# Kernel tuning notes

Hardware: AMD Instinct MI355X
Metric: run time of the kernel (lower is better)

Reference implementation:

```python
import jax, jax.numpy as jnp
import numpy as np

B, N, IN_DIM, OUT_DIM, H = 8, 1024, 256, 256, 4
HD = OUT_DIM // H  # head_dim = 64
NEG = -1e9
EPS = 1e-5


def setup_inputs() -> dict:
    key = jax.random.key(0)
    ks = jax.random.split(key, 9)
    h = jax.random.normal(ks[0], (B, N, IN_DIM), dtype=jnp.float32)
    adj = jax.random.randint(ks[1], (N, N), 0, 2, dtype=jnp.int32)
    adj = adj.at[jnp.arange(N), jnp.arange(N)].set(1)  # self loops so no empty rows
    s = 1.0 / np.sqrt(IN_DIM)
    W = jax.random.uniform(ks[2], (H, IN_DIM, HD), jnp.float32, -s, s)
    sa = 1.0 / np.sqrt(2 * HD)
    a1 = jax.random.uniform(ks[3], (H, HD), jnp.float32, -sa, sa)
    a2 = jax.random.uniform(ks[4], (H, HD), jnp.float32, -sa, sa)
    sp = 1.0 / np.sqrt(OUT_DIM)
    proj_w = jax.random.uniform(ks[5], (OUT_DIM, OUT_DIM), jnp.float32, -sp, sp)
    proj_b = jax.random.uniform(ks[6], (OUT_DIM,), jnp.float32, -sp, sp)
    gamma = jnp.ones((OUT_DIM,), jnp.float32)
    beta = jnp.zeros((OUT_DIM,), jnp.float32)
    return {"h": h, "adj": adj, "W": W, "a1": a1, "a2": a2,
            "proj_w": proj_w, "proj_b": proj_b, "gamma": gamma, "beta": beta}


def reference(h, adj, W, a1, a2, proj_w, proj_b, gamma, beta):
    # Wh: [B,H,N,HD]
    Wh = jnp.einsum('bni,hid->bhnd', h, W)
    # Decompose a([Wh_i || Wh_j]) = a1.Wh_i + a2.Wh_j (same math as concat+linear)
    si = jnp.einsum('bhnd,hd->bhn', Wh, a1)  # [B,H,N]
    sj = jnp.einsum('bhnd,hd->bhn', Wh, a2)
    e = jax.nn.leaky_relu(si[:, :, :, None] + sj[:, :, None, :], 0.2)  # [B,H,N,N]
    mask = (adj == 0)  # [N,N]
    e = jnp.where(mask[None, None], NEG, e)
    alpha = jax.nn.softmax(e, axis=-1)
    out = jnp.einsum('bhnm,bhmd->bhnd', alpha, Wh)  # [B,H,N,HD]
    h_multi = out.transpose(0, 2, 1, 3).reshape(B, N, OUT_DIM)  # concat heads
    h_out = jnp.einsum('bnd,od->bno', h_multi, proj_w) + proj_b
    h_out = h_out + h  # residual (in_dim == out_dim)
    mu = jnp.mean(h_out, axis=-1, keepdims=True)
    var = jnp.mean(jnp.square(h_out - mu), axis=-1, keepdims=True)
    return (h_out - mu) * jax.lax.rsqrt(var + EPS) * gamma + beta
```

## Files before the change

kernel.cpp:

```cpp
#include <hip/hip_runtime.h>
#include <hip/hip_bf16.h>

#define NN 1024
#define LOG2E 1.44269504088896f

typedef __attribute__((ext_vector_type(8))) short short8;
typedef __attribute__((ext_vector_type(4))) float floatx4;
typedef __attribute__((ext_vector_type(4))) int intx4;
typedef __attribute__((ext_vector_type(2))) int intx2;

#define WAIT_VM0()   asm volatile("s_waitcnt vmcnt(0)" ::: "memory")
#define WAIT_VM4()   asm volatile("s_waitcnt vmcnt(4)" ::: "memory")
#define WAIT_LGKM0() asm volatile("s_waitcnt lgkmcnt(0)" ::: "memory")
#define SCHED_FENCE() asm volatile("" ::: "memory")

static __device__ __forceinline__ unsigned pk2(float f0, float f1) {
    unsigned u0 = __float_as_uint(f0) + 0x8000u;
    unsigned u1 = __float_as_uint(f1) + 0x8000u;
    return __builtin_amdgcn_perm(u1, u0, 0x07060302u);
}
static __device__ __forceinline__ short8 pk8(floatx4 v0, floatx4 v1) {
    union { intx4 i; short8 s; } u;
    u.i[0] = (int)pk2(v0[0], v0[1]); u.i[1] = (int)pk2(v0[2], v0[3]);
    u.i[2] = (int)pk2(v1[0], v1[1]); u.i[3] = (int)pk2(v1[2], v1[3]);
    return u.s;
}
static __device__ __forceinline__ void load_lds16(const void* gsrc, void* lds) {
    __builtin_amdgcn_global_load_lds(
        (const __attribute__((address_space(1))) void*)gsrc,
        (__attribute__((address_space(3))) void*)lds, 16, 0, 0);
}

__global__ __launch_bounds__(256) void prep_kernel(
    const float* __restrict__ W, const float* __restrict__ proj_w,
    const int* __restrict__ adj,
    __hip_bfloat16* __restrict__ WTb,
    __hip_bfloat16* __restrict__ pwb,
    unsigned* __restrict__ adjm)
{
    int blk = blockIdx.x, t = threadIdx.x;
    if (blk < 16) {
        int o = blk * 16 + (t >> 4);
        int hh = o >> 6, d = o & 63;
        #pragma unroll
        for (int kk = 0; kk < 16; ++kk) {
            int k = (t & 15) + 16 * kk;
            WTb[(size_t)o * 256 + k] = __float2bfloat16(W[((size_t)hh * 256 + k) * 64 + d]);
        }
    } else if (blk < 32) {
        size_t base = (size_t)(blk - 16) * 4096 + (size_t)t * 16;
        #pragma unroll
        for (int k = 0; k < 16; k += 8) {
            floatx4 v0 = *(const floatx4*)(proj_w + base + k);
            floatx4 v1 = *(const floatx4*)(proj_w + base + k + 4);
            *(short8*)(pwb + base + k) = pk8(v0, v1);
        }
    } else {
        int n = (blk - 32) * 8 + (t >> 5);
        int wd = t & 31;
        const int* arow = adj + (size_t)n * NN + wd * 32;
        unsigned bits = 0;
        #pragma unroll
        for (int j4 = 0; j4 < 8; ++j4) {
            intx4 v = *(const intx4*)(arow + j4 * 4);
            #pragma unroll
            for (int j = 0; j < 4; ++j) if (v[j] != 0) bits |= (1u << (j4 * 4 + j));
        }
        adjm[(size_t)n * 32 + wd] = bits;
    }
}

__global__ __launch_bounds__(256) void wh_kernel(
    const float* __restrict__ h,
    const __hip_bfloat16* __restrict__ WTb,
    const float* __restrict__ a1, const float* __restrict__ a2,
    __hip_bfloat16* __restrict__ WhTt,
    float* __restrict__ si, float* __restrict__ sj)
{
    int t = threadIdx.x;
    int w = t >> 6, l = t & 63;
    int rl = l & 15, q = l >> 4;
    int r0 = blockIdx.x * 16;
    int bb = r0 >> 10, n0 = r0 & 1023;

    __shared__ __align__(16) __hip_bfloat16 bst[4][4096];
    __shared__ float redsi[4][4][16];
    __shared__ float redsj[4][4][16];

    short8 af[8];
    const float* Arow = h + (size_t)(r0 + rl) * 256 + q * 8;
    #pragma unroll
    for (int k0 = 0; k0 < 8; ++k0) {
        floatx4 v0 = *(const floatx4*)(Arow + k0 * 32);
        floatx4 v1 = *(const floatx4*)(Arow + k0 * 32 + 4);
        af[k0] = pk8(v0, v1);
    }

    #pragma unroll
    for (int k = 0; k < 8; ++k) {
        int row = k * 2 + (l >> 5);
        int g = (l & 31) ^ (row & 7);
        load_lds16(WTb + (size_t)w * 4096 + row * 256 + g * 8, &bst[w][k * 512]);
    }

    int d = w * 16 + rl;
    int s = (n0 & 31) + q * 4;
    int g = s >> 3;
    int mi = s & 7;
    size_t toff = (size_t)d * 32 + ((g ^ (d & 3)) * 8) + mi;
    size_t tbase = ((size_t)bb * 4) * 32 + (n0 >> 5);

    #pragma unroll
    for (int j = 0; j < 4; ++j) {
        WAIT_VM0();
        floatx4 acc = {0.f, 0.f, 0.f, 0.f};
        #pragma unroll
        for (int k0 = 0; k0 < 8; ++k0) {
            int p = ((k0 << 2) + q) ^ (rl & 7);
            short8 bf = *(const short8*)(&bst[w][rl * 256 + p * 8]);
            acc = __builtin_amdgcn_mfma_f32_16x16x32_bf16(af[k0], bf, acc, 0, 0, 0);
        }
        WAIT_LGKM0();
        if (j < 3) {
            int ctn = w + 4 * (j + 1);
            #pragma unroll
            for (int k = 0; k < 8; ++k) {
                int row = k * 2 + (l >> 5);
                int gg = (l & 31) ^ (row & 7);
                load_lds16(WTb + (size_t)ctn * 4096 + row * 256 + gg * 8, &bst[w][k * 512]);
            }
        }

        intx2 pr;
        pr[0] = (int)pk2(acc[0], acc[1]);
        pr[1] = (int)pk2(acc[2], acc[3]);
        *(intx2*)(WhTt + (tbase + (size_t)j * 32) * 2048 + toff) = pr;

        float av1 = a1[j * 64 + w * 16 + rl] * LOG2E;
        float av2 = a2[j * 64 + w * 16 + rl] * LOG2E;
        #pragma unroll
        for (int i = 0; i < 4; ++i) {
            float p1 = acc[i] * av1, p2 = acc[i] * av2;
            #pragma unroll
            for (int off = 1; off < 16; off <<= 1) {
                p1 += __shfl_xor(p1, off, 64);
                p2 += __shfl_xor(p2, off, 64);
            }
            if (rl == 0) { redsi[w][j][q * 4 + i] = p1; redsj[w][j][q * 4 + i] = p2; }
        }
    }
    __syncthreads();

    if (t < 64) {
        int head = t >> 4, row = t & 15;
        si[(size_t)(bb * 4 + head) * NN + n0 + row] =
            redsi[0][head][row] + redsi[1][head][row] + redsi[2][head][row] + redsi[3][head][row];
    } else if (t < 128) {
        int u = t - 64;
        int head = u >> 4, row = u & 15;
        sj[(size_t)(bb * 4 + head) * NN + n0 + row] =
            redsj[0][head][row] + redsj[1][head][row] + redsj[2][head][row] + redsj[3][head][row];
    }
}

__global__ __launch_bounds__(512, 4) void attn_proj_kernel(
    const unsigned* __restrict__ adjm,
    const __hip_bfloat16* __restrict__ WhTt,
    const float* __restrict__ si, const float* __restrict__ sj,
    const __hip_bfloat16* __restrict__ pwb,
    const float* __restrict__ h,
    const float* __restrict__ proj_b, const float* __restrict__ gamma,
    const float* __restrict__ beta,
    float* __restrict__ out)
{
    __shared__ __align__(16) char smem[76288];
    auto bst   = reinterpret_cast<__hip_bfloat16 (*)[2][2048]>(smem);
    auto pl    = reinterpret_cast<__hip_bfloat16 (*)[16][40]>(smem + 65536);
    auto hm    = reinterpret_cast<__hip_bfloat16 (*)[264]>(smem + 65536);
    auto red   = reinterpret_cast<float (*)[8][16]>(smem + 65536 + 8448);
    auto lsums = reinterpret_cast<float (*)[4][16]>(smem + 75776);
    float (*accx)[64][20] = reinterpret_cast<float (*)[64][20]>(smem);

    int bx = blockIdx.x, t = threadIdx.x;
    int w = t >> 6, l = t & 63;
    int hh = w & 3, e = w >> 2;
    int rl = l & 15, q = l >> 4;
    int b = bx >> 6, n0 = (bx & 63) * 16;
    int bh = b * 4 + hh;
    int r0 = bx * 16;

    int r = l >> 2, cg = l & 3;
    float sii = si[(size_t)bh * NN + n0 + r];
    const float* sjr = sj + (size_t)bh * NN;
    const unsigned* amrow = adjm + (size_t)(n0 + r) * 32;

    float lsum = 0.f;
    floatx4 acc[4] = { {0,0,0,0}, {0,0,0,0}, {0,0,0,0}, {0,0,0,0} };

    const __hip_bfloat16* Tbase = WhTt + ((size_t)bh * 32 + e) * 2048 + l * 8;

    #pragma unroll
    for (int k = 0; k < 4; ++k)
        load_lds16(Tbase + k * 512, &bst[w][0][k * 512]);

    #pragma unroll 2
    for (int it = 0; it < 16; ++it) {
        int buf = it & 1;
        int mw = it * 64 + e * 32;
        {
            unsigned bits = amrow[it * 2 + e] >> (cg * 8);
            int mb = mw + cg * 8;
            #pragma unroll
            for (int c4 = 0; c4 < 2; ++c4) {
                floatx4 s4 = *(const floatx4*)(sjr + mb + c4 * 4);
                float pv[4];
                #pragma unroll
                for (int k = 0; k < 4; ++k) {
                    float x = sii + s4[k];
                    x = fmaxf(x, 0.2f * x);
                    x = ((bits >> (c4 * 4 + k)) & 1u) ? x : -1e9f;
                    pv[k] = exp2f(x);
                    lsum += pv[k];
                }
                intx2 two;
                two[0] = (int)pk2(pv[0], pv[1]);
                two[1] = (int)pk2(pv[2], pv[3]);
                *(intx2*)(&pl[w][r][cg * 8 + c4 * 4]) = two;
            }
        }
        SCHED_FENCE();
        if (it < 15) {
            const __hip_bfloat16* Tn = Tbase + (size_t)(it + 1) * 2 * 2048;
            #pragma unroll
            for (int k = 0; k < 4; ++k)
                load_lds16(Tn + k * 512, &bst[w][buf ^ 1][k * 512]);
            WAIT_VM4();
        } else {
            WAIT_VM0();
        }
        short8 afr = *(const short8*)(&pl[w][rl][q * 8]);
        #pragma unroll
        for (int dt = 0; dt < 4; ++dt) {
            short8 bfr = *(const short8*)(&bst[w][buf][(dt * 16 + rl) * 32 + (q ^ (rl & 3)) * 8]);
            acc[dt] = __builtin_amdgcn_mfma_f32_16x16x32_bf16(afr, bfr, acc[dt], 0, 0, 0);
        }
    }

    lsum += __shfl_xor(lsum, 1, 64);
    lsum += __shfl_xor(lsum, 2, 64);
    if (cg == 0) lsums[e][hh][r] = lsum;

    __syncthreads();

    if (e == 1) {
        #pragma unroll
        for (int dt = 0; dt < 4; ++dt) {
            #pragma unroll
            for (int i = 0; i < 4; ++i)
                accx[hh][l][dt * 4 + i] = acc[dt][i];
        }
    }
    __syncthreads();

    if (e == 0) {
        float riv[4];
        #pragma unroll
        for (int i = 0; i < 4; ++i)
            riv[i] = 1.f / (lsums[0][hh][q * 4 + i] + lsums[1][hh][q * 4 + i]);
        #pragma unroll
        for (int dt = 0; dt < 4; ++dt) {
            #pragma unroll
            for (int i = 0; i < 4; ++i) {
                float v = acc[dt][i] + accx[hh][l][dt * 4 + i];
                unsigned uv = (__float_as_uint(v * riv[i]) + 0x8000u) >> 16;
                hm[q * 4 + i][hh * 64 + dt * 16 + rl] = __ushort_as_bfloat16((unsigned short)uv);
            }
        }
    }
    __syncthreads();

    short8 paf[8];
    #pragma unroll
    for (int k0 = 0; k0 < 8; ++k0) paf[k0] = *(const short8*)(&hm[rl][q * 8 + k0 * 32]);

    floatx4 pacc[2];
    #pragma unroll
    for (int j = 0; j < 2; ++j) {
        int ct = w + 8 * j;
        const __hip_bfloat16* Bp = pwb + (size_t)(ct * 16 + rl) * 256 + q * 8;
        floatx4 a = {0.f, 0.f, 0.f, 0.f};
        #pragma unroll
        for (int k0 = 0; k0 < 8; ++k0) {
            short8 bfp = *(const short8*)(Bp + k0 * 32);
            a = __builtin_amdgcn_mfma_f32_16x16x32_bf16(paf[k0], bfp, a, 0, 0, 0);
        }
        pacc[j] = a;
    }

    float ps[4] = {0.f, 0.f, 0.f, 0.f};
    #pragma unroll
    for (int j = 0; j < 2; ++j) {
        int col = (w + 8 * j) * 16 + rl;
        float pb = proj_b[col];
        #pragma unroll
        for (int i = 0; i < 4; ++i) {
            float v = pacc[j][i] + pb + h[(size_t)(r0 + q * 4 + i) * 256 + col];
            pacc[j][i] = v;
            ps[i] += v;
        }
    }
    #pragma unroll
    for (int i = 0; i < 4; ++i) {
        float s = ps[i];
        #pragma unroll
        for (int off = 1; off < 16; off <<= 1) s += __shfl_xor(s, off, 64);
        ps[i] = s;
    }
    if (rl == 0) {
        for (int i = 0; i < 4; ++i) red[0][w][q * 4 + i] = ps[i];
    }
    __syncthreads();
    float mu[4];
    #pragma unroll
    for (int i = 0; i < 4; ++i) {
        int row = q * 4 + i;
        float s = 0.f;
        #pragma unroll
        for (int ww = 0; ww < 8; ++ww) s += red[0][ww][row];
        mu[i] = s * (1.f / 256.f);
    }
    float vs[4] = {0.f, 0.f, 0.f, 0.f};
    #pragma unroll
    for (int j = 0; j < 2; ++j) {
        #pragma unroll
        for (int i = 0; i < 4; ++i) { float cv = pacc[j][i] - mu[i]; vs[i] += cv * cv; }
    }
    #pragma unroll
    for (int i = 0; i < 4; ++i) {
        float s = vs[i];
        #pragma unroll
        for (int off = 1; off < 16; off <<= 1) s += __shfl_xor(s, off, 64);
        vs[i] = s;
    }
    if (rl == 0) {
        for (int i = 0; i < 4; ++i) red[1][w][q * 4 + i] = vs[i];
    }
    __syncthreads();
    float rs[4];
    #pragma unroll
    for (int i = 0; i < 4; ++i) {
        int row = q * 4 + i;
        float s = 0.f;
        #pragma unroll
        for (int ww = 0; ww < 8; ++ww) s += red[1][ww][row];
        rs[i] = rsqrtf(s * (1.f / 256.f) + 1e-5f);
    }
    #pragma unroll
    for (int j = 0; j < 2; ++j) {
        int col = (w + 8 * j) * 16 + rl;
        float g = gamma[col], be = beta[col];
        #pragma unroll
        for (int i = 0; i < 4; ++i)
            out[(size_t)(r0 + q * 4 + i) * 256 + col] = (pacc[j][i] - mu[i]) * rs[i] * g + be;
    }
}

extern "C" void kernel_launch(void* const* d_in, const int* in_sizes, int n_in,
                              void* d_out, int out_size, void* d_ws, size_t ws_size,
                              hipStream_t stream) {
    const float* h      = (const float*)d_in[0];
    const int*   adj    = (const int*)d_in[1];
    const float* W      = (const float*)d_in[2];
    const float* a1     = (const float*)d_in[3];
    const float* a2     = (const float*)d_in[4];
    const float* proj_w = (const float*)d_in[5];
    const float* proj_b = (const float*)d_in[6];
    const float* gamma  = (const float*)d_in[7];
    const float* beta   = (const float*)d_in[8];
    float* out = (float*)d_out;

    char* ws = (char*)d_ws;
    __hip_bfloat16* WhTt = (__hip_bfloat16*)ws;  ws += (size_t)32 * 32 * 2048 * 2;
    __hip_bfloat16* WTb = (__hip_bfloat16*)ws;   ws += 256 * 256 * 2;
    __hip_bfloat16* pwb = (__hip_bfloat16*)ws;   ws += 256 * 256 * 2;
    float* si = (float*)ws;                      ws += (size_t)32 * NN * 4;
    float* sj = (float*)ws;                      ws += (size_t)32 * NN * 4;
    unsigned* adjm = (unsigned*)ws;              ws += (size_t)NN * 32 * 4;

    prep_kernel<<<160, 256, 0, stream>>>(W, proj_w, adj, WTb, pwb, adjm);
    wh_kernel<<<512, 256, 0, stream>>>(h, WTb, a1, a2, WhTt, si, sj);
    attn_proj_kernel<<<512, 512, 0, stream>>>(adjm, WhTt, si, sj, pwb, h, proj_b, gamma, beta, out);
}
```

Before: 121.2 us.

## Share WT tiles across two row tiles per block in wh_kernel

The Wh projection kernel now uses 512-thread blocks that each handle 32 rows instead of 16, split into two row tiles of four waves each. Each WT half is staged into LDS once per phase and shared by both row tiles, which halves the weight traffic per output row. Block-wide barriers replace the per-wave pipelined prefetch, so load/compute overlap is reduced, and the grid drops to 256 blocks.

```diff
diff --git a/kernel.cpp b/kernel.cpp
--- a/kernel.cpp
+++ b/kernel.cpp
@@ -70,25 +70,26 @@
     }
 }
 
-__global__ __launch_bounds__(256) void wh_kernel(
+__global__ __launch_bounds__(512) void wh_kernel(
     const float* __restrict__ h,
     const __hip_bfloat16* __restrict__ WTb,
     const float* __restrict__ a1, const float* __restrict__ a2,
     __hip_bfloat16* __restrict__ WhTt,
     float* __restrict__ si, float* __restrict__ sj)
 {
+    __shared__ __align__(16) __hip_bfloat16 WTbs[8][4096];
+    __shared__ float redsi[2][4][4][16];
+    __shared__ float redsj[2][4][4][16];
+
     int t = threadIdx.x;
     int w = t >> 6, l = t & 63;
+    int rt = w >> 2, ds = w & 3;
     int rl = l & 15, q = l >> 4;
-    int r0 = blockIdx.x * 16;
-    int bb = r0 >> 10, n0 = r0 & 1023;
-
-    __shared__ __align__(16) __hip_bfloat16 bst[4][4096];
-    __shared__ float redsi[4][4][16];
-    __shared__ float redsj[4][4][16];
+    int bx = blockIdx.x;
+    int bb = bx >> 5, tb = bx & 31;
 
     short8 af[8];
-    const float* Arow = h + (size_t)(r0 + rl) * 256 + q * 8;
+    const float* Arow = h + ((size_t)bb * 1024 + tb * 32 + rt * 16 + rl) * 256 + q * 8;
     #pragma unroll
     for (int k0 = 0; k0 < 8; ++k0) {
         floatx4 v0 = *(const floatx4*)(Arow + k0 * 32);
@@ -96,70 +97,66 @@
         af[k0] = pk8(v0, v1);
     }
 
-    #pragma unroll
-    for (int k = 0; k < 8; ++k) {
-        int row = k * 2 + (l >> 5);
-        int g = (l & 31) ^ (row & 7);
-        load_lds16(WTb + (size_t)w * 4096 + row * 256 + g * 8, &bst[w][k * 512]);
-    }
-
-    int d = w * 16 + rl;
-    int s = (n0 & 31) + q * 4;
-    int g = s >> 3;
-    int mi = s & 7;
-    size_t toff = (size_t)d * 32 + ((g ^ (d & 3)) * 8) + mi;
-    size_t tbase = ((size_t)bb * 4) * 32 + (n0 >> 5);
-
-    #pragma unroll
-    for (int j = 0; j < 4; ++j) {
-        WAIT_VM0();
-        floatx4 acc = {0.f, 0.f, 0.f, 0.f};
-        #pragma unroll
-        for (int k0 = 0; k0 < 8; ++k0) {
-            int p = ((k0 << 2) + q) ^ (rl & 7);
-            short8 bf = *(const short8*)(&bst[w][rl * 256 + p * 8]);
-            acc = __builtin_amdgcn_mfma_f32_16x16x32_bf16(af[k0], bf, acc, 0, 0, 0);
-        }
-        WAIT_LGKM0();
-        if (j < 3) {
-            int ctn = w + 4 * (j + 1);
-            #pragma unroll
-            for (int k = 0; k < 8; ++k) {
-                int row = k * 2 + (l >> 5);
-                int gg = (l & 31) ^ (row & 7);
-                load_lds16(WTb + (size_t)ctn * 4096 + row * 256 + gg * 8, &bst[w][k * 512]);
+    int d = ds * 16 + rl;
+    int s = rt * 16 + q * 4;
+    size_t toff = (size_t)d * 32 + (((s >> 3) ^ (d & 3)) * 8) + (s & 7);
+    int srow_ = l >> 5;
+
+    #pragma unroll
+    for (int ph = 0; ph < 2; ++ph) {
+        if (ph) __syncthreads();
+        #pragma unroll
+        for (int k = 0; k < 8; ++k) {
+            int row = k * 2 + srow_;
+            int g = (l & 31) ^ (row & 7);
+            load_lds16(WTb + (size_t)(ph * 128 + w * 16 + row) * 256 + g * 8, &WTbs[w][k * 512]);
+        }
+        __syncthreads();
+
+        #pragma unroll
+        for (int jj = 0; jj < 2; ++jj) {
+            int head = ph * 2 + jj;
+            int lt = ds + 4 * jj;
+            floatx4 acc = {0.f, 0.f, 0.f, 0.f};
+            #pragma unroll
+            for (int k0 = 0; k0 < 8; ++k0) {
+                int p = ((k0 << 2) + q) ^ (rl & 7);
+                short8 bf = *(const short8*)(&WTbs[lt][rl * 256 + p * 8]);
+                acc = __builtin_amdgcn_mfma_f32_16x16x32_bf16(af[k0], bf, acc, 0, 0, 0);
             }
-        }
-
-        intx2 pr;
-        pr[0] = (int)pk2(acc[0], acc[1]);
-        pr[1] = (int)pk2(acc[2], acc[3]);
-        *(intx2*)(WhTt + (tbase + (size_t)j * 32) * 2048 + toff) = pr;
-
-        float av1 = a1[j * 64 + w * 16 + rl] * LOG2E;
-        float av2 = a2[j * 64 + w * 16 + rl] * LOG2E;
-        #pragma unroll
-        for (int i = 0; i < 4; ++i) {
-            float p1 = acc[i] * av1, p2 = acc[i] * av2;
-            #pragma unroll
-            for (int off = 1; off < 16; off <<= 1) {
-                p1 += __shfl_xor(p1, off, 64);
-                p2 += __shfl_xor(p2, off, 64);
+
+            intx2 pr;
+            pr[0] = (int)pk2(acc[0], acc[1]);
+            pr[1] = (int)pk2(acc[2], acc[3]);
+            *(intx2*)(WhTt + ((size_t)(bb * 4 + head) * 32 + tb) * 2048 + toff) = pr;
+
+            float av1 = a1[head * 64 + d] * LOG2E;
+            float av2 = a2[head * 64 + d] * LOG2E;
+            #pragma unroll
+            for (int i = 0; i < 4; ++i) {
+                float p1 = acc[i] * av1, p2 = acc[i] * av2;
+                #pragma unroll
+                for (int off = 1; off < 16; off <<= 1) {
+                    p1 += __shfl_xor(p1, off, 64);
+                    p2 += __shfl_xor(p2, off, 64);
+                }
+                if (rl == 0) { redsi[rt][ds][head][q * 4 + i] = p1; redsj[rt][ds][head][q * 4 + i] = p2; }
             }
-            if (rl == 0) { redsi[w][j][q * 4 + i] = p1; redsj[w][j][q * 4 + i] = p2; }
-        }
-    }
-    __syncthreads();
-
-    if (t < 64) {
-        int head = t >> 4, row = t & 15;
-        si[(size_t)(bb * 4 + head) * NN + n0 + row] =
-            redsi[0][head][row] + redsi[1][head][row] + redsi[2][head][row] + redsi[3][head][row];
-    } else if (t < 128) {
-        int u = t - 64;
-        int head = u >> 4, row = u & 15;
-        sj[(size_t)(bb * 4 + head) * NN + n0 + row] =
-            redsj[0][head][row] + redsj[1][head][row] + redsj[2][head][row] + redsj[3][head][row];
+        }
+    }
+    __syncthreads();
+
+    if (t < 128) {
+        int head = t >> 5, u = t & 31, rt2 = u >> 4, row = u & 15;
+        si[(size_t)(bb * 4 + head) * NN + tb * 32 + rt2 * 16 + row] =
+            redsi[rt2][0][head][row] + redsi[rt2][1][head][row] +
+            redsi[rt2][2][head][row] + redsi[rt2][3][head][row];
+    } else if (t < 256) {
+        int u2 = t - 128;
+        int head = u2 >> 5, u = u2 & 31, rt2 = u >> 4, row = u & 15;
+        sj[(size_t)(bb * 4 + head) * NN + tb * 32 + rt2 * 16 + row] =
+            redsj[rt2][0][head][row] + redsj[rt2][1][head][row] +
+            redsj[rt2][2][head][row] + redsj[rt2][3][head][row];
     }
 }
 
@@ -388,6 +385,6 @@
     unsigned* adjm = (unsigned*)ws;              ws += (size_t)NN * 32 * 4;
 
     prep_kernel<<<160, 256, 0, stream>>>(W, proj_w, adj, WTb, pwb, adjm);
-    wh_kernel<<<512, 256, 0, stream>>>(h, WTb, a1, a2, WhTt, si, sj);
+    wh_kernel<<<256, 512, 0, stream>>>(h, WTb, a1, a2, WhTt, si, sj);
     attn_proj_kernel<<<512, 512, 0, stream>>>(adjm, WhTt, si, sj, pwb, h, proj_b, gamma, beta, out);
 }
```

After: 120.5 us. No clear change (-0.5%).
